# Kernel tuning notes

Hardware: AMD Instinct MI355X
Metric: run time of the kernel (lower is better)

Reference implementation:

```python
import jax, jax.numpy as jnp
import numpy as np

B, D, H = 2048, 32, 512  # batch, state dim (x has D+1 cols incl. logdet slot), MLP hidden


def setup_inputs() -> dict:
    key = jax.random.key(0)
    ks = jax.random.split(key, 6)
    return {
        "t": jax.random.uniform(ks[0], (1,), dtype=jnp.float32),
        "x": jax.random.normal(ks[1], (B, D + 1), dtype=jnp.float32),
        "W1": jax.random.normal(ks[2], (D + 1, H), dtype=jnp.float32) / np.float32(np.sqrt(D + 1)),
        "b1": jnp.zeros((H,), jnp.float32),
        "W2": jax.random.normal(ks[3], (H, H), dtype=jnp.float32) / np.float32(np.sqrt(H)),
        "b2": jnp.zeros((H,), jnp.float32),
        "W3": jax.random.normal(ks[4], (H, D), dtype=jnp.float32) / np.float32(np.sqrt(H)),
        "b3": jnp.zeros((D,), jnp.float32),
    }


def _vf_single(xi, t, W1, b1, W2, b2, W3, b3):
    # single-sample vector field: R^D -> R^D, time t concatenated as a feature
    inp = jnp.concatenate([xi, t])  # (D+1,)
    h = jnp.tanh(inp @ W1 + b1)
    h = jnp.tanh(h @ W2 + b2)
    return h @ W3 + b3


def reference(t, x, W1, b1, W2, b2, W3, b3):
    xs = x[..., :-1]  # (B, D): drop logdet accumulator column
    # batched vector field dx = vf(t, xs)
    tt = jnp.broadcast_to(t, (xs.shape[0], 1))
    inp = jnp.concatenate([xs, tt], axis=-1)  # (B, D+1)
    h = jnp.tanh(inp @ W1 + b1)
    h = jnp.tanh(h @ W2 + b2)
    dx = h @ W3 + b3  # (B, D)
    # exact divergence: trace of per-sample Jacobian (torch vmap(jacrev) equivalent)
    f = lambda xi: _vf_single(xi, t, W1, b1, W2, b2, W3, b3)
    div = jax.vmap(lambda xi: jnp.trace(jax.jacfwd(f)(xi)))(xs)  # (B,)
    return jnp.concatenate([dx, div[:, None]], axis=-1)  # (B, D+1)
```

## Files before the change

kernel.cpp:

```cpp
#include <hip/hip_runtime.h>
#include <math.h>

constexpr int NB = 2048;
constexpr int ND = 32;
constexpr int NH = 512;
constexpr int NKI = NH / 32;

typedef __bf16 bf16x8 __attribute__((ext_vector_type(8)));
typedef float floatx4 __attribute__((ext_vector_type(4)));

__device__ inline float fast_tanh(float x) {
  float e = __expf(2.f * x);
  return 1.f - 2.f / (e + 1.f);
}


__global__ __launch_bounds__(256) void k_pre(
    const float* __restrict__ x, const float* __restrict__ t,
    const float* __restrict__ W1, const float* __restrict__ b1,
    const float* __restrict__ W2, const float* __restrict__ W3,
    __bf16* __restrict__ H1p, __bf16* __restrict__ D1p,
    __bf16* __restrict__ W2p, __bf16* __restrict__ Mp,
    float* __restrict__ W3T, float* __restrict__ out) {
  if (blockIdx.x < 512) {
    int gid = blockIdx.x * 256 + threadIdx.x;
    if (gid < NB * (ND + 1)) out[gid] = 0.f;
    int lane = gid & 63;
    int ki = (gid >> 6) & (NKI - 1);
    int rt = gid >> 10;
    int m = rt * 16 + (lane & 15);
    int k0 = ki * 32 + (lane >> 4) * 8;
    const float* xs = x + m * (ND + 1);

    float acc[8];
#pragma unroll
    for (int j = 0; j < 8; ++j) acc[j] = b1[k0 + j];
#pragma unroll
    for (int i = 0; i < ND; ++i) {
      float xv = xs[i];
      float4 u = *(const float4*)&W1[i * NH + k0];
      float4 v = *(const float4*)&W1[i * NH + k0 + 4];
      acc[0] += xv * u.x; acc[1] += xv * u.y;
      acc[2] += xv * u.z; acc[3] += xv * u.w;
      acc[4] += xv * v.x; acc[5] += xv * v.y;
      acc[6] += xv * v.z; acc[7] += xv * v.w;
    }
    {
      float tv = t[0];
      float4 u = *(const float4*)&W1[ND * NH + k0];
      float4 v = *(const float4*)&W1[ND * NH + k0 + 4];
      acc[0] += tv * u.x; acc[1] += tv * u.y;
      acc[2] += tv * u.z; acc[3] += tv * u.w;
      acc[4] += tv * v.x; acc[5] += tv * v.y;
      acc[6] += tv * v.z; acc[7] += tv * v.w;
    }
    __bf16 hv[8], dv[8];
#pragma unroll
    for (int j = 0; j < 8; ++j) {
      float h = fast_tanh(acc[j]);
      hv[j] = (__bf16)h;
      dv[j] = (__bf16)(1.f - h * h);
    }
    long off = (long)gid * 8;
    *(bf16x8*)(H1p + off) = *(bf16x8*)hv;
    *(bf16x8*)(D1p + off) = *(bf16x8*)dv;
  } else {
    int pb = blockIdx.x - 512;
    int gid2 = pb * 256 + threadIdx.x;
    if (gid2 < ND * NH)
      W3T[gid2] = W3[(gid2 & (NH - 1)) * ND + (gid2 >> 9)];

    bool doM = pb >= 128;
    int gid = (pb & 127) * 256 + threadIdx.x;
    int lane = gid & 63;
    int ki = (gid >> 6) & (NKI - 1);
    int ct = gid >> 10;
    int n = ct * 16 + (lane & 15);
    int k0 = ki * 32 + (lane >> 4) * 8;
    long off = (long)gid * 8;

    if (!doM) {
      __bf16 v[8];
#pragma unroll
      for (int j = 0; j < 8; ++j) v[j] = (__bf16)W2[(k0 + j) * NH + n];
      *(bf16x8*)(W2p + off) = *(bf16x8*)v;
    } else {
      float acc[8];
#pragma unroll
      for (int j = 0; j < 8; ++j) acc[j] = 0.f;
      for (int i = 0; i < ND; ++i) {
        float w3 = W3[n * ND + i];
        float4 u = *(const float4*)&W1[i * NH + k0];
        float4 v = *(const float4*)&W1[i * NH + k0 + 4];
        acc[0] += w3 * u.x; acc[1] += w3 * u.y;
        acc[2] += w3 * u.z; acc[3] += w3 * u.w;
        acc[4] += w3 * v.x; acc[5] += w3 * v.y;
        acc[6] += w3 * v.z; acc[7] += w3 * v.w;
      }
      __bf16 v[8];
#pragma unroll
      for (int j = 0; j < 8; ++j)
        v[j] = (__bf16)(W2[(k0 + j) * NH + n] * acc[j]);
      *(bf16x8*)(Mp + off) = *(bf16x8*)v;
    }
  }
}

__global__ __launch_bounds__(256) void k_main(
    const __bf16* __restrict__ Ah, const __bf16* __restrict__ Ad,
    const __bf16* __restrict__ W2p, const __bf16* __restrict__ Mp,
    const float* __restrict__ b2, const float* __restrict__ W3T,
    const float* __restrict__ b3, float* __restrict__ out) {
  __shared__ float h2s[16][260];
  __shared__ float divred[4][16];

  int bid = blockIdx.x;
  int rt = bid >> 1;
  int half = bid & 1;
  int tid = threadIdx.x;
  int w = tid >> 6, lane = tid & 63;
  int col = lane & 15, quad = lane >> 4;
  int ct0 = half * 16 + w * 4;

  floatx4 accH[4] = {{0,0,0,0},{0,0,0,0},{0,0,0,0},{0,0,0,0}};
  floatx4 accM[4] = {{0,0,0,0},{0,0,0,0},{0,0,0,0},{0,0,0,0}};
  long abase = (long)rt * NKI;
#pragma unroll 2
  for (int ki = 0; ki < NKI; ++ki) {
    bf16x8 ah = *(const bf16x8*)(Ah + ((abase + ki) * 64 + lane) * 8);
    bf16x8 ad = *(const bf16x8*)(Ad + ((abase + ki) * 64 + lane) * 8);
#pragma unroll
    for (int c = 0; c < 4; ++c) {
      long boff = ((long)((ct0 + c) * NKI + ki) * 64 + lane) * 8;
      bf16x8 bw = *(const bf16x8*)(W2p + boff);
      bf16x8 bm = *(const bf16x8*)(Mp + boff);
      accH[c] = __builtin_amdgcn_mfma_f32_16x16x32_bf16(ah, bw, accH[c], 0, 0, 0);
      accM[c] = __builtin_amdgcn_mfma_f32_16x16x32_bf16(ad, bm, accM[c], 0, 0, 0);
    }
  }

  float divv[4] = {0.f, 0.f, 0.f, 0.f};
#pragma unroll
  for (int c = 0; c < 4; ++c) {
    int n = (ct0 + c) * 16 + col;
    int nc = (w * 4 + c) * 16 + col;
    float bb = b2[n];
#pragma unroll
    for (int r = 0; r < 4; ++r) {
      float h2 = fast_tanh(accH[c][r] + bb);
      h2s[quad * 4 + r][nc] = h2;
      divv[r] += accM[c][r] * (1.f - h2 * h2);
    }
  }
#pragma unroll
  for (int r = 0; r < 4; ++r) {
    float v = divv[r];
    v += __shfl_xor(v, 1);
    v += __shfl_xor(v, 2);
    v += __shfl_xor(v, 4);
    v += __shfl_xor(v, 8);
    if (col == 0) divred[w][quad * 4 + r] = v;
  }
  __syncthreads();
  if (tid < 16) {
    float v = divred[0][tid] + divred[1][tid] + divred[2][tid] + divred[3][tid];
    atomicAdd(&out[(rt * 16 + tid) * (ND + 1) + ND], v);
  }

  int row = tid & 15;
  int i0 = tid >> 4;
  const float* w3a = W3T + (long)(i0 * 2 + 0) * NH + half * 256;
  const float* w3b = W3T + (long)(i0 * 2 + 1) * NH + half * 256;
  float a0 = 0.f, a1 = 0.f;
#pragma unroll 4
  for (int kk = 0; kk < 256; kk += 4) {
    float4 h = *(const float4*)&h2s[row][kk];
    float4 wa = *(const float4*)&w3a[kk];
    float4 wb = *(const float4*)&w3b[kk];
    a0 += h.x * wa.x + h.y * wa.y + h.z * wa.z + h.w * wa.w;
    a1 += h.x * wb.x + h.y * wb.y + h.z * wb.z + h.w * wb.w;
  }
  if (half == 0) { a0 += b3[i0 * 2]; a1 += b3[i0 * 2 + 1]; }
  float* orow = out + (long)(rt * 16 + row) * (ND + 1);
  atomicAdd(&orow[i0 * 2], a0);
  atomicAdd(&orow[i0 * 2 + 1], a1);
}

extern "C" void kernel_launch(void* const* d_in, const int* in_sizes, int n_in,
                              void* d_out, int out_size, void* d_ws, size_t ws_size,
                              hipStream_t stream) {
  const float* t  = (const float*)d_in[0];
  const float* x  = (const float*)d_in[1];
  const float* W1 = (const float*)d_in[2];
  const float* b1 = (const float*)d_in[3];
  const float* W2 = (const float*)d_in[4];
  const float* b2 = (const float*)d_in[5];
  const float* W3 = (const float*)d_in[6];
  const float* b3 = (const float*)d_in[7];
  float* out = (float*)d_out;

  __bf16* W2p = (__bf16*)d_ws;
  __bf16* Mp  = W2p + NH * NH;
  __bf16* H1p = Mp + NH * NH;
  __bf16* D1p = H1p + NB * NH;
  float*  W3T = (float*)(D1p + NB * NH);

  k_pre<<<768, 256, 0, stream>>>(x, t, W1, b1, W2, W3, H1p, D1p, W2p, Mp, W3T, out);
  k_main<<<256, 256, 0, stream>>>(H1p, D1p, W2p, Mp, b2, W3T, b3, out);
}
```

Baseline: 109.4 us.

## Fuse first-layer tanh computation into main kernel via shared memory

After: 104.7 us. 1.04x faster.

```diff
diff --git a/kernel.cpp b/kernel.cpp
--- a/kernel.cpp
+++ b/kernel.cpp
@@ -7,6 +7,7 @@
 constexpr int NKI = NH / 32;
 
 typedef __bf16 bf16x8 __attribute__((ext_vector_type(8)));
+typedef __bf16 bf16x4 __attribute__((ext_vector_type(4)));
 typedef float floatx4 __attribute__((ext_vector_type(4)));
 
 __device__ inline float fast_tanh(float x) {
@@ -16,101 +17,59 @@
 
 
 __global__ __launch_bounds__(256) void k_pre(
+    const float* __restrict__ W1, const float* __restrict__ W2,
+    const float* __restrict__ W3, __bf16* __restrict__ W2p,
+    __bf16* __restrict__ Mp, float* __restrict__ W3T,
+    float* __restrict__ out) {
+  int g = blockIdx.x * 256 + threadIdx.x;
+  for (int idx = g; idx < NB * (ND + 1); idx += 65536) out[idx] = 0.f;
+  if (g < ND * NH)
+    W3T[g] = W3[(g & (NH - 1)) * ND + (g >> 9)];
+
+  bool doM = blockIdx.x >= 128;
+  int gid = (blockIdx.x & 127) * 256 + threadIdx.x;
+  int lane = gid & 63;
+  int ki = (gid >> 6) & (NKI - 1);
+  int ct = gid >> 10;
+  int n = ct * 16 + (lane & 15);
+  int k0 = ki * 32 + (lane >> 4) * 8;
+  long off = (long)gid * 8;
+
+  if (!doM) {
+    __bf16 v[8];
+#pragma unroll
+    for (int j = 0; j < 8; ++j) v[j] = (__bf16)W2[(k0 + j) * NH + n];
+    *(bf16x8*)(W2p + off) = *(bf16x8*)v;
+  } else {
+    float acc[8];
+#pragma unroll
+    for (int j = 0; j < 8; ++j) acc[j] = 0.f;
+    for (int i = 0; i < ND; ++i) {
+      float w3 = W3[n * ND + i];
+      float4 u = *(const float4*)&W1[i * NH + k0];
+      float4 v = *(const float4*)&W1[i * NH + k0 + 4];
+      acc[0] += w3 * u.x; acc[1] += w3 * u.y;
+      acc[2] += w3 * u.z; acc[3] += w3 * u.w;
+      acc[4] += w3 * v.x; acc[5] += w3 * v.y;
+      acc[6] += w3 * v.z; acc[7] += w3 * v.w;
+    }
+    __bf16 v[8];
+#pragma unroll
+    for (int j = 0; j < 8; ++j)
+      v[j] = (__bf16)(W2[(k0 + j) * NH + n] * acc[j]);
+    *(bf16x8*)(Mp + off) = *(bf16x8*)v;
+  }
+}
+
+__global__ __launch_bounds__(256) void k_main(
     const float* __restrict__ x, const float* __restrict__ t,
     const float* __restrict__ W1, const float* __restrict__ b1,
-    const float* __restrict__ W2, const float* __restrict__ W3,
-    __bf16* __restrict__ H1p, __bf16* __restrict__ D1p,
-    __bf16* __restrict__ W2p, __bf16* __restrict__ Mp,
-    float* __restrict__ W3T, float* __restrict__ out) {
-  if (blockIdx.x < 512) {
-    int gid = blockIdx.x * 256 + threadIdx.x;
-    if (gid < NB * (ND + 1)) out[gid] = 0.f;
-    int lane = gid & 63;
-    int ki = (gid >> 6) & (NKI - 1);
-    int rt = gid >> 10;
-    int m = rt * 16 + (lane & 15);
-    int k0 = ki * 32 + (lane >> 4) * 8;
-    const float* xs = x + m * (ND + 1);
-
-    float acc[8];
-#pragma unroll
-    for (int j = 0; j < 8; ++j) acc[j] = b1[k0 + j];
-#pragma unroll
-    for (int i = 0; i < ND; ++i) {
-      float xv = xs[i];
-      float4 u = *(const float4*)&W1[i * NH + k0];
-      float4 v = *(const float4*)&W1[i * NH + k0 + 4];
-      acc[0] += xv * u.x; acc[1] += xv * u.y;
-      acc[2] += xv * u.z; acc[3] += xv * u.w;
-      acc[4] += xv * v.x; acc[5] += xv * v.y;
-      acc[6] += xv * v.z; acc[7] += xv * v.w;
-    }
-    {
-      float tv = t[0];
-      float4 u = *(const float4*)&W1[ND * NH + k0];
-      float4 v = *(const float4*)&W1[ND * NH + k0 + 4];
-      acc[0] += tv * u.x; acc[1] += tv * u.y;
-      acc[2] += tv * u.z; acc[3] += tv * u.w;
-      acc[4] += tv * v.x; acc[5] += tv * v.y;
-      acc[6] += tv * v.z; acc[7] += tv * v.w;
-    }
-    __bf16 hv[8], dv[8];
-#pragma unroll
-    for (int j = 0; j < 8; ++j) {
-      float h = fast_tanh(acc[j]);
-      hv[j] = (__bf16)h;
-      dv[j] = (__bf16)(1.f - h * h);
-    }
-    long off = (long)gid * 8;
-    *(bf16x8*)(H1p + off) = *(bf16x8*)hv;
-    *(bf16x8*)(D1p + off) = *(bf16x8*)dv;
-  } else {
-    int pb = blockIdx.x - 512;
-    int gid2 = pb * 256 + threadIdx.x;
-    if (gid2 < ND * NH)
-      W3T[gid2] = W3[(gid2 & (NH - 1)) * ND + (gid2 >> 9)];
-
-    bool doM = pb >= 128;
-    int gid = (pb & 127) * 256 + threadIdx.x;
-    int lane = gid & 63;
-    int ki = (gid >> 6) & (NKI - 1);
-    int ct = gid >> 10;
-    int n = ct * 16 + (lane & 15);
-    int k0 = ki * 32 + (lane >> 4) * 8;
-    long off = (long)gid * 8;
-
-    if (!doM) {
-      __bf16 v[8];
-#pragma unroll
-      for (int j = 0; j < 8; ++j) v[j] = (__bf16)W2[(k0 + j) * NH + n];
-      *(bf16x8*)(W2p + off) = *(bf16x8*)v;
-    } else {
-      float acc[8];
-#pragma unroll
-      for (int j = 0; j < 8; ++j) acc[j] = 0.f;
-      for (int i = 0; i < ND; ++i) {
-        float w3 = W3[n * ND + i];
-        float4 u = *(const float4*)&W1[i * NH + k0];
-        float4 v = *(const float4*)&W1[i * NH + k0 + 4];
-        acc[0] += w3 * u.x; acc[1] += w3 * u.y;
-        acc[2] += w3 * u.z; acc[3] += w3 * u.w;
-        acc[4] += w3 * v.x; acc[5] += w3 * v.y;
-        acc[6] += w3 * v.z; acc[7] += w3 * v.w;
-      }
-      __bf16 v[8];
-#pragma unroll
-      for (int j = 0; j < 8; ++j)
-        v[j] = (__bf16)(W2[(k0 + j) * NH + n] * acc[j]);
-      *(bf16x8*)(Mp + off) = *(bf16x8*)v;
-    }
-  }
-}
-
-__global__ __launch_bounds__(256) void k_main(
-    const __bf16* __restrict__ Ah, const __bf16* __restrict__ Ad,
     const __bf16* __restrict__ W2p, const __bf16* __restrict__ Mp,
     const float* __restrict__ b2, const float* __restrict__ W3T,
     const float* __restrict__ b3, float* __restrict__ out) {
+  __shared__ __bf16 aH[16 * NH];
+  __shared__ __bf16 aD[16 * NH];
+  __shared__ float xs[16][36];
   __shared__ float h2s[16][260];
   __shared__ float divred[4][16];
 
@@ -118,17 +77,57 @@
   int rt = bid >> 1;
   int half = bid & 1;
   int tid = threadIdx.x;
+
+  for (int idx = tid; idx < 16 * 33; idx += 256) {
+    int r = idx / 33, i = idx - r * 33;
+    xs[r][i] = x[(rt * 16 + r) * (ND + 1) + i];
+  }
+  float tv = t[0];
+  __syncthreads();
+
+  {
+    int r = tid >> 4;
+    int cb = (tid & 15) * 4;
+#pragma unroll
+    for (int it = 0; it < 8; ++it) {
+      int c0 = cb + it * 64;
+      float4 bb = *(const float4*)&b1[c0];
+      float a0 = bb.x, a1 = bb.y, a2 = bb.z, a3 = bb.w;
+#pragma unroll
+      for (int i = 0; i < ND; ++i) {
+        float xv = xs[r][i];
+        float4 w = *(const float4*)&W1[i * NH + c0];
+        a0 += xv * w.x; a1 += xv * w.y; a2 += xv * w.z; a3 += xv * w.w;
+      }
+      {
+        float4 w = *(const float4*)&W1[ND * NH + c0];
+        a0 += tv * w.x; a1 += tv * w.y; a2 += tv * w.z; a3 += tv * w.w;
+      }
+      float h0 = fast_tanh(a0), h1 = fast_tanh(a1);
+      float h2 = fast_tanh(a2), h3 = fast_tanh(a3);
+      __bf16 hv[4] = {(__bf16)h0, (__bf16)h1, (__bf16)h2, (__bf16)h3};
+      __bf16 dv[4] = {(__bf16)(1.f - h0 * h0), (__bf16)(1.f - h1 * h1),
+                      (__bf16)(1.f - h2 * h2), (__bf16)(1.f - h3 * h3)};
+      int ki = c0 >> 5;
+      int lane = r | (((c0 >> 3) & 3) << 4);
+      int j = c0 & 7;
+      int ofs = (ki * 64 + lane) * 8 + j;
+      *(bf16x4*)(aH + ofs) = *(bf16x4*)hv;
+      *(bf16x4*)(aD + ofs) = *(bf16x4*)dv;
+    }
+  }
+  __syncthreads();
+
   int w = tid >> 6, lane = tid & 63;
   int col = lane & 15, quad = lane >> 4;
   int ct0 = half * 16 + w * 4;
 
   floatx4 accH[4] = {{0,0,0,0},{0,0,0,0},{0,0,0,0},{0,0,0,0}};
   floatx4 accM[4] = {{0,0,0,0},{0,0,0,0},{0,0,0,0},{0,0,0,0}};
-  long abase = (long)rt * NKI;
 #pragma unroll 2
   for (int ki = 0; ki < NKI; ++ki) {
-    bf16x8 ah = *(const bf16x8*)(Ah + ((abase + ki) * 64 + lane) * 8);
-    bf16x8 ad = *(const bf16x8*)(Ad + ((abase + ki) * 64 + lane) * 8);
+    bf16x8 ah = *(const bf16x8*)(aH + (ki * 64 + lane) * 8);
+    bf16x8 ad = *(const bf16x8*)(aD + (ki * 64 + lane) * 8);
 #pragma unroll
     for (int c = 0; c < 4; ++c) {
       long boff = ((long)((ct0 + c) * NKI + ki) * 64 + lane) * 8;
@@ -201,10 +200,8 @@
 
   __bf16* W2p = (__bf16*)d_ws;
   __bf16* Mp  = W2p + NH * NH;
-  __bf16* H1p = Mp + NH * NH;
-  __bf16* D1p = H1p + NB * NH;
-  float*  W3T = (float*)(D1p + NB * NH);
-
-  k_pre<<<768, 256, 0, stream>>>(x, t, W1, b1, W2, W3, H1p, D1p, W2p, Mp, W3T, out);
-  k_main<<<256, 256, 0, stream>>>(H1p, D1p, W2p, Mp, b2, W3T, b3, out);
-}
+  float*  W3T = (float*)(Mp + NH * NH);
+
+  k_pre<<<256, 256, 0, stream>>>(W1, W2, W3, W2p, Mp, W3T, out);
+  k_main<<<256, 256, 0, stream>>>(x, t, W1, b1, W2p, Mp, b2, W3T, b3, out);
+}
```
